# Optimization experiments

Hardware: AMD Instinct MI355X
Metric: run time of the kernel (lower is better)

The kernel has to match this reference:

```python
import jax, jax.numpy as jnp
import numpy as np

N_ATOMS = 200000
AEV_DIM = 384
H1, H2, H3 = 160, 128, 96
N_SPECIES = 4
ALPHA = 0.1  # CELU alpha used by ANI atomic networks


def setup_inputs() -> dict:
    key = jax.random.key(0)
    ks = jax.random.split(key, 8)
    aev = jax.random.normal(ks[0], (N_ATOMS, AEV_DIM), dtype=jnp.float32)
    # Disjoint species partition (matches (species==s).nonzero() buffers)
    perm = jax.random.permutation(ks[1], N_ATOMS)
    chunk = N_ATOMS // N_SPECIES
    H_idx = perm[0 * chunk:1 * chunk]
    C_idx = perm[1 * chunk:2 * chunk]
    N_idx = perm[2 * chunk:3 * chunk]
    O_idx = perm[3 * chunk:4 * chunk]

    def init(k, shape, fan_in):
        return (jax.random.normal(k, shape, dtype=jnp.float32) / np.float32(np.sqrt(fan_in)))

    # Stacked per-species MLP params: leading axis = species (H,C,N,O)
    W1 = init(ks[2], (N_SPECIES, AEV_DIM, H1), AEV_DIM); b1 = jnp.zeros((N_SPECIES, H1), jnp.float32)
    W2 = init(ks[3], (N_SPECIES, H1, H2), H1);          b2 = jnp.zeros((N_SPECIES, H2), jnp.float32)
    W3 = init(ks[4], (N_SPECIES, H2, H3), H2);          b3 = jnp.zeros((N_SPECIES, H3), jnp.float32)
    W4 = init(ks[5], (N_SPECIES, H3, 1), H3);           b4 = jnp.zeros((N_SPECIES, 1), jnp.float32)
    return {"aev": aev,
            "W1": W1, "b1": b1, "W2": W2, "b2": b2,
            "W3": W3, "b3": b3, "W4": W4, "b4": b4,
            "H_idx": H_idx, "C_idx": C_idx, "N_idx": N_idx, "O_idx": O_idx}


def _species_mlp(x, W1, b1, W2, b2, W3, b3, W4, b4):
    h = jax.nn.celu(x @ W1 + b1, ALPHA)
    h = jax.nn.celu(h @ W2 + b2, ALPHA)
    h = jax.nn.celu(h @ W3 + b3, ALPHA)
    return (h @ W4 + b4).reshape(-1)  # per-atom scalar energy


def reference(aev, W1, b1, W2, b2, W3, b3, W4, b4, H_idx, C_idx, N_idx, O_idx):
    out = jnp.zeros((aev.shape[0],), dtype=aev.dtype)
    # Fixed small loop over the 4 species networks (structurally distinct experts)
    for s, idx in enumerate((H_idx, C_idx, N_idx, O_idx)):
        e = _species_mlp(aev[idx], W1[s], b1[s], W2[s], b2[s], W3[s], b3[s], W4[s], b4[s])
        out = out.at[idx].add(e)  # index_add_ scatter
    # output.unsqueeze(0).sum(dim=1) -> molecular energy, shape [1]
    return out[None, :].sum(axis=1)
```

## Files before the change

kernel.cpp:

```cpp
#include <hip/hip_runtime.h>

#define DI __device__ __forceinline__

constexpr int AEV = 384;
constexpr int H1N = 160;
constexpr int H2N = 128;
constexpr int H3N = 96;
constexpr int NSP = 4;
constexpr int W1P = 200;
constexpr int W2P = 168;
constexpr int W3P = 136;
constexpr int W3OFF = H2N * W2P;

using half8  = __attribute__((ext_vector_type(8))) _Float16;
using half4v = __attribute__((ext_vector_type(4))) _Float16;
using f32x4  = __attribute__((ext_vector_type(4))) float;

__device__ __align__(16) _Float16 g_w1[NSP * H1N * AEV];
__device__ __align__(16) _Float16 g_w2[NSP * H2N * H1N];
__device__ __align__(16) _Float16 g_w3[NSP * H3N * H2N];

DI float celu_f(float x) {
  return fmaxf(x, 0.f) + 0.1f * (exp2f(fminf(x, 0.f) * 14.426950408889634f) - 1.f);
}
DI f32x4 mfma16h(half8 a, half8 b, f32x4 c) {
  return __builtin_amdgcn_mfma_f32_16x16x32_f16(a, b, c, 0, 0, 0);
}
DI half8 cvt8(float4 a, float4 b) {
  half8 t;
  t[0] = (_Float16)a.x; t[1] = (_Float16)a.y; t[2] = (_Float16)a.z; t[3] = (_Float16)a.w;
  t[4] = (_Float16)b.x; t[5] = (_Float16)b.y; t[6] = (_Float16)b.z; t[7] = (_Float16)b.w;
  return t;
}
DI half4v shfl4(half4v v, int src) {
  union { half4v h; int i[2]; } u;
  u.h = v;
  u.i[0] = __shfl(u.i[0], src, 64);
  u.i[1] = __shfl(u.i[1], src, 64);
  return u.h;
}
DI half8 bfrag(const half4v* hb, int ks, int l15, int quad) {
  const int sLo = (quad & 1) * 32 + l15, sHi = sLo + 16;
  half4v loA = shfl4(hb[2 * ks], sLo),     loB = shfl4(hb[2 * ks + 1], sLo);
  half4v hiA = shfl4(hb[2 * ks], sHi),     hiB = shfl4(hb[2 * ks + 1], sHi);
  half4v lo = (quad & 2) ? loB : loA;
  half4v hi = (quad & 2) ? hiB : hiA;
  half8 b;
  b[0] = lo[0]; b[1] = lo[1]; b[2] = lo[2]; b[3] = lo[3];
  b[4] = hi[0]; b[5] = hi[1]; b[6] = hi[2]; b[7] = hi[3];
  return b;
}

template <int K, int N>
DI void tp(const float* __restrict__ src, _Float16* dst, int id) {
  constexpr int per = K * N;
  int s = id / per, r = id % per;
  int n = r / K, k = r % K;
  dst[s * per + n * K + k] = (_Float16)src[s * per + k * N + n];
}

__global__ void prep(const float* __restrict__ W1, const float* __restrict__ W2,
                     const float* __restrict__ W3, float* __restrict__ out) {
  int id = blockIdx.x * 256 + threadIdx.x;
  if (id == 0) out[0] = 0.f;
  constexpr int E1 = NSP * AEV * H1N;
  constexpr int E2 = NSP * H1N * H2N;
  constexpr int E3 = NSP * H2N * H3N;
  if (id < E1)                 tp<AEV, H1N>(W1, g_w1, id);
  else if (id < E1 + E2)       tp<H1N, H2N>(W2, g_w2, id - E1);
  else if (id < E1 + E2 + E3)  tp<H2N, H3N>(W3, g_w3, id - E1 - E2);
}

__global__ __launch_bounds__(512, 4) void fused_mlp(
    const float* __restrict__ aev,
    const float* __restrict__ b1, const float* __restrict__ b2,
    const float* __restrict__ b3,
    const float* __restrict__ W4, const float* __restrict__ pb4,
    const int* __restrict__ i0, const int* __restrict__ i1,
    const int* __restrict__ i2, const int* __restrict__ i3,
    int chunk, float* __restrict__ out) {
  __shared__ __align__(16) _Float16 WS[34560];
  __shared__ float RED[8];

  const int tid  = threadIdx.x;
  const int lane = tid & 63, wav = tid >> 6;
  const int l15  = lane & 15, quad = lane >> 4;
  const int s    = blockIdx.y;
  const int* idx = (s == 0) ? i0 : (s == 1) ? i1 : (s == 2) ? i2 : i3;

  const int a = blockIdx.x * 128 + wav * 16 + l15;
  const bool valid = (a < chunk);
  const int r = idx[valid ? a : (chunk - 1)];
  const float* xr = aev + (size_t)r * AEV + quad * 8;

  const _Float16* w1src = g_w1 + (size_t)s * H1N * AEV;

#pragma unroll
  for (int i = 0; i < 8; ++i) {
    int c = tid + i * 512;
    if (c < H1N * 24) {
      int n = c / 24, kc = c % 24;
      *(half8*)(WS + n * W1P + kc * 8) = *(const half8*)(w1src + n * AEV + kc * 8);
    }
  }
  __syncthreads();

  f32x4 acc[10];
#pragma unroll
  for (int m = 0; m < 10; ++m)
#pragma unroll
    for (int i = 0; i < 4; ++i) acc[m][i] = 0.f;

  float4 xf0 = *(const float4*)(xr), xf1 = *(const float4*)(xr + 4);
#pragma unroll
  for (int ks = 0; ks < 6; ++ks) {
    half8 bv = cvt8(xf0, xf1);
    xf0 = *(const float4*)(xr + (ks + 1) * 32);
    xf1 = *(const float4*)(xr + (ks + 1) * 32 + 4);
#pragma unroll
    for (int mt = 0; mt < 10; ++mt) {
      half8 aw = *(const half8*)(WS + (mt * 16 + l15) * W1P + ks * 32 + quad * 8);
      acc[mt] = mfma16h(aw, bv, acc[mt]);
    }
  }
  __syncthreads();
#pragma unroll
  for (int i = 0; i < 8; ++i) {
    int c = tid + i * 512;
    if (c < H1N * 24) {
      int n = c / 24, kc = c % 24;
      *(half8*)(WS + n * W1P + kc * 8) = *(const half8*)(w1src + 192 + n * AEV + kc * 8);
    }
  }
  __syncthreads();
#pragma unroll
  for (int ks = 6; ks < 12; ++ks) {
    half8 bv = cvt8(xf0, xf1);
    if (ks < 11) {
      xf0 = *(const float4*)(xr + (ks + 1) * 32);
      xf1 = *(const float4*)(xr + (ks + 1) * 32 + 4);
    }
#pragma unroll
    for (int mt = 0; mt < 10; ++mt) {
      half8 aw = *(const half8*)(WS + (mt * 16 + l15) * W1P + (ks - 6) * 32 + quad * 8);
      acc[mt] = mfma16h(aw, bv, acc[mt]);
    }
  }
  half4v hb[10];
#pragma unroll
  for (int mt = 0; mt < 10; ++mt) {
    float4 bb = *(const float4*)(b1 + s * H1N + mt * 16 + quad * 4);
    half4v o;
    o[0] = (_Float16)celu_f(acc[mt][0] + bb.x);
    o[1] = (_Float16)celu_f(acc[mt][1] + bb.y);
    o[2] = (_Float16)celu_f(acc[mt][2] + bb.z);
    o[3] = (_Float16)celu_f(acc[mt][3] + bb.w);
    hb[mt] = o;
  }

  __syncthreads();
  {
    const _Float16* w2src = g_w2 + (size_t)s * H2N * H1N;
    const _Float16* w3src = g_w3 + (size_t)s * H3N * H2N;
#pragma unroll
    for (int i = 0; i < 5; ++i) {
      int c = tid + i * 512;
      int n = c / 20, kc = c % 20;
      *(half8*)(WS + n * W2P + kc * 8) = *(const half8*)(w2src + n * H1N + kc * 8);
    }
#pragma unroll
    for (int i = 0; i < 3; ++i) {
      int c = tid + i * 512;
      int n = c / 16, kc = c % 16;
      *(half8*)(WS + W3OFF + n * W3P + kc * 8) = *(const half8*)(w3src + n * H2N + kc * 8);
    }
  }
  __syncthreads();

  f32x4 acc2[8];
#pragma unroll
  for (int m = 0; m < 8; ++m)
#pragma unroll
    for (int i = 0; i < 4; ++i) acc2[m][i] = 0.f;
#pragma unroll
  for (int ks = 0; ks < 5; ++ks) {
    half8 bv = bfrag(hb, ks, l15, quad);
#pragma unroll
    for (int mt = 0; mt < 8; ++mt) {
      half8 aw = *(const half8*)(WS + (mt * 16 + l15) * W2P + ks * 32 + quad * 8);
      acc2[mt] = mfma16h(aw, bv, acc2[mt]);
    }
  }
  half4v hb2[8];
#pragma unroll
  for (int mt = 0; mt < 8; ++mt) {
    float4 bb = *(const float4*)(b2 + s * H2N + mt * 16 + quad * 4);
    half4v o;
    o[0] = (_Float16)celu_f(acc2[mt][0] + bb.x);
    o[1] = (_Float16)celu_f(acc2[mt][1] + bb.y);
    o[2] = (_Float16)celu_f(acc2[mt][2] + bb.z);
    o[3] = (_Float16)celu_f(acc2[mt][3] + bb.w);
    hb2[mt] = o;
  }

  f32x4 acc3[6];
#pragma unroll
  for (int m = 0; m < 6; ++m)
#pragma unroll
    for (int i = 0; i < 4; ++i) acc3[m][i] = 0.f;
#pragma unroll
  for (int ks = 0; ks < 4; ++ks) {
    half8 bv = bfrag(hb2, ks, l15, quad);
#pragma unroll
    for (int mt = 0; mt < 6; ++mt) {
      half8 aw = *(const half8*)(WS + W3OFF + (mt * 16 + l15) * W3P + ks * 32 + quad * 8);
      acc3[mt] = mfma16h(aw, bv, acc3[mt]);
    }
  }

  float e = 0.f;
#pragma unroll
  for (int mt = 0; mt < 6; ++mt) {
    float4 bb = *(const float4*)(b3 + s * H3N + mt * 16 + quad * 4);
    float4 wv = *(const float4*)(W4 + s * H3N + mt * 16 + quad * 4);
    e += (float)(_Float16)celu_f(acc3[mt][0] + bb.x) * wv.x
       + (float)(_Float16)celu_f(acc3[mt][1] + bb.y) * wv.y
       + (float)(_Float16)celu_f(acc3[mt][2] + bb.z) * wv.z
       + (float)(_Float16)celu_f(acc3[mt][3] + bb.w) * wv.w;
  }
  e += __shfl_xor(e, 16, 64);
  e += __shfl_xor(e, 32, 64);
  e = (lane < 16 && valid) ? (e + pb4[s]) : 0.f;
#pragma unroll
  for (int off = 1; off < 64; off <<= 1) e += __shfl_xor(e, off, 64);
  if (lane == 0) RED[wav] = e;
  __syncthreads();
  if (tid == 0) {
    float t = 0.f;
#pragma unroll
    for (int i = 0; i < 8; ++i) t += RED[i];
    atomicAdd(out, t);
  }
}

extern "C" void kernel_launch(void* const* d_in, const int* in_sizes, int n_in,
                              void* d_out, int out_size, void* d_ws, size_t ws_size,
                              hipStream_t stream) {
  (void)n_in; (void)d_ws; (void)ws_size; (void)out_size;
  const float* aev = (const float*)d_in[0];
  const float* W1  = (const float*)d_in[1];
  const float* b1  = (const float*)d_in[2];
  const float* W2  = (const float*)d_in[3];
  const float* b2  = (const float*)d_in[4];
  const float* W3  = (const float*)d_in[5];
  const float* b3  = (const float*)d_in[6];
  const float* W4  = (const float*)d_in[7];
  const float* b4  = (const float*)d_in[8];
  const int* iH = (const int*)d_in[9];
  const int* iC = (const int*)d_in[10];
  const int* iN = (const int*)d_in[11];
  const int* iO = (const int*)d_in[12];
  const int chunk = in_sizes[9];

  constexpr int TOT = NSP * (AEV * H1N + H1N * H2N + H2N * H3N);
  prep<<<TOT / 256, 256, 0, stream>>>(W1, W2, W3, (float*)d_out);

  const int tiles = (chunk + 127) / 128;
  fused_mlp<<<dim3(tiles, NSP), 512, 0, stream>>>(aev, b1, b2, b3, W4, b4,
                                                  iH, iC, iN, iO, chunk, (float*)d_out);
}
```

Before: 477.5 us.

## Make MLP kernel persistent with resident W1 and cross-tile AEV prefetch

Switches to a persistent grid of 64 blocks per species that loop over 128-atom tiles. The full W1 slice stays resident in LDS for the whole block. W2 and W3 are restaged in a shared region each iteration. The next tile's AEV rows are prefetched with nontemporal loads during layers 2-3, and the atomic add happens once per block. This removes the per-tile W1 reload, the launch overhead, and the exposed gather latency. In exchange it drops occupancy to 2 blocks per CU, adds more barriers per tile, and reloads W2/W3 from global memory every tile.

```diff
diff --git a/kernel.cpp b/kernel.cpp
--- a/kernel.cpp
+++ b/kernel.cpp
@@ -7,10 +7,13 @@
 constexpr int H2N = 128;
 constexpr int H3N = 96;
 constexpr int NSP = 4;
-constexpr int W1P = 200;
-constexpr int W2P = 168;
-constexpr int W3P = 136;
-constexpr int W3OFF = H2N * W2P;
+
+constexpr int W1P  = 392;
+constexpr int W2AP = 104;
+constexpr int W2BP = 72;
+constexpr int W3P  = 136;
+constexpr int RH   = H1N * W1P;
+constexpr int WSH  = RH + H2N * W2AP;
 
 using half8  = __attribute__((ext_vector_type(8))) _Float16;
 using half4v = __attribute__((ext_vector_type(4))) _Float16;
@@ -26,10 +29,10 @@
 DI f32x4 mfma16h(half8 a, half8 b, f32x4 c) {
   return __builtin_amdgcn_mfma_f32_16x16x32_f16(a, b, c, 0, 0, 0);
 }
-DI half8 cvt8(float4 a, float4 b) {
+DI half8 cvt8(f32x4 a, f32x4 b) {
   half8 t;
-  t[0] = (_Float16)a.x; t[1] = (_Float16)a.y; t[2] = (_Float16)a.z; t[3] = (_Float16)a.w;
-  t[4] = (_Float16)b.x; t[5] = (_Float16)b.y; t[6] = (_Float16)b.z; t[7] = (_Float16)b.w;
+  t[0] = (_Float16)a[0]; t[1] = (_Float16)a[1]; t[2] = (_Float16)a[2]; t[3] = (_Float16)a[3];
+  t[4] = (_Float16)b[0]; t[5] = (_Float16)b[1]; t[6] = (_Float16)b[2]; t[7] = (_Float16)b[3];
   return t;
 }
 DI half4v shfl4(half4v v, int src) {
@@ -50,6 +53,7 @@
   b[4] = hi[0]; b[5] = hi[1]; b[6] = hi[2]; b[7] = hi[3];
   return b;
 }
+DI f32x4 ntl4(const float* p) { return __builtin_nontemporal_load((const f32x4*)p); }
 
 template <int K, int N>
 DI void tp(const float* __restrict__ src, _Float16* dst, int id) {
@@ -71,7 +75,7 @@
   else if (id < E1 + E2 + E3)  tp<H2N, H3N>(W3, g_w3, id - E1 - E2);
 }
 
-__global__ __launch_bounds__(512, 4) void fused_mlp(
+__global__ __launch_bounds__(512, 2) void fused_mlp(
     const float* __restrict__ aev,
     const float* __restrict__ b1, const float* __restrict__ b2,
     const float* __restrict__ b3,
@@ -79,7 +83,7 @@
     const int* __restrict__ i0, const int* __restrict__ i1,
     const int* __restrict__ i2, const int* __restrict__ i3,
     int chunk, float* __restrict__ out) {
-  __shared__ __align__(16) _Float16 WS[34560];
+  __shared__ __align__(16) _Float16 WS[WSH];
   __shared__ float RED[8];
 
   const int tid  = threadIdx.x;
@@ -87,160 +91,188 @@
   const int l15  = lane & 15, quad = lane >> 4;
   const int s    = blockIdx.y;
   const int* idx = (s == 0) ? i0 : (s == 1) ? i1 : (s == 2) ? i2 : i3;
-
-  const int a = blockIdx.x * 128 + wav * 16 + l15;
-  const bool valid = (a < chunk);
-  const int r = idx[valid ? a : (chunk - 1)];
-  const float* xr = aev + (size_t)r * AEV + quad * 8;
+  const int ntiles = (chunk + 127) >> 7;
 
   const _Float16* w1src = g_w1 + (size_t)s * H1N * AEV;
-
-#pragma unroll
-  for (int i = 0; i < 8; ++i) {
+  const _Float16* w2src = g_w2 + (size_t)s * H2N * H1N;
+  const _Float16* w3src = g_w3 + (size_t)s * H3N * H2N;
+
+#pragma unroll
+  for (int i = 0; i < 15; ++i) {
     int c = tid + i * 512;
-    if (c < H1N * 24) {
-      int n = c / 24, kc = c % 24;
-      *(half8*)(WS + n * W1P + kc * 8) = *(const half8*)(w1src + n * AEV + kc * 8);
-    }
+    int n = c / 48, kc = c % 48;
+    *(half8*)(WS + n * W1P + kc * 8) = *(const half8*)(w1src + n * AEV + kc * 8);
   }
+
+  int t = blockIdx.x;
+  bool valid;
+  const float* xr;
+  {
+    int a = t * 128 + wav * 16 + l15;
+    valid = (a < chunk);
+    int r = idx[valid ? a : (chunk - 1)];
+    xr = aev + (size_t)r * AEV + quad * 8;
+  }
+  f32x4 pA0 = ntl4(xr),      pB0 = ntl4(xr + 4);
+  f32x4 pA1 = ntl4(xr + 32), pB1 = ntl4(xr + 36);
+  f32x4 pA2 = ntl4(xr + 64), pB2 = ntl4(xr + 68);
+  f32x4 pA3 = ntl4(xr + 96), pB3 = ntl4(xr + 100);
+
+  float bsum = 0.f;
   __syncthreads();
 
-  f32x4 acc[10];
-#pragma unroll
-  for (int m = 0; m < 10; ++m)
-#pragma unroll
-    for (int i = 0; i < 4; ++i) acc[m][i] = 0.f;
-
-  float4 xf0 = *(const float4*)(xr), xf1 = *(const float4*)(xr + 4);
-#pragma unroll
-  for (int ks = 0; ks < 6; ++ks) {
-    half8 bv = cvt8(xf0, xf1);
-    xf0 = *(const float4*)(xr + (ks + 1) * 32);
-    xf1 = *(const float4*)(xr + (ks + 1) * 32 + 4);
+  for (; t < ntiles; t += 64) {
+    f32x4 acc[10];
+#pragma unroll
+    for (int m = 0; m < 10; ++m)
+#pragma unroll
+      for (int i = 0; i < 4; ++i) acc[m][i] = 0.f;
+#pragma unroll
+    for (int ks = 0; ks < 12; ++ks) {
+      half8 bv = cvt8(pA0, pB0);
+      pA0 = pA1; pB0 = pB1; pA1 = pA2; pB1 = pB2; pA2 = pA3; pB2 = pB3;
+      if (ks < 8) {
+        pA3 = ntl4(xr + (ks + 4) * 32);
+        pB3 = ntl4(xr + (ks + 4) * 32 + 4);
+      }
+#pragma unroll
+      for (int mt = 0; mt < 10; ++mt) {
+        half8 aw = *(const half8*)(WS + (mt * 16 + l15) * W1P + ks * 32 + quad * 8);
+        acc[mt] = mfma16h(aw, bv, acc[mt]);
+      }
+    }
+    half4v hb[10];
 #pragma unroll
     for (int mt = 0; mt < 10; ++mt) {
-      half8 aw = *(const half8*)(WS + (mt * 16 + l15) * W1P + ks * 32 + quad * 8);
-      acc[mt] = mfma16h(aw, bv, acc[mt]);
-    }
+      float4 bb = *(const float4*)(b1 + s * H1N + mt * 16 + quad * 4);
+      half4v o;
+      o[0] = (_Float16)celu_f(acc[mt][0] + bb.x);
+      o[1] = (_Float16)celu_f(acc[mt][1] + bb.y);
+      o[2] = (_Float16)celu_f(acc[mt][2] + bb.z);
+      o[3] = (_Float16)celu_f(acc[mt][3] + bb.w);
+      hb[mt] = o;
+    }
+
+    bool v2;
+    const float* xr2;
+    {
+      int a2 = (t + 64) * 128 + wav * 16 + l15;
+      v2 = (a2 < chunk);
+      int r2 = idx[v2 ? a2 : (chunk - 1)];
+      xr2 = aev + (size_t)r2 * AEV + quad * 8;
+    }
+    const int nA0 = tid / 12,          kA0 = tid % 12;
+    const int nA1 = (tid + 512) / 12,  kA1 = (tid + 512) % 12;
+    const int nA2 = (tid + 1024) / 12, kA2 = (tid + 1024) % 12;
+    half8 sA0 = *(const half8*)(w2src + nA0 * H1N + kA0 * 8);
+    half8 sA1 = *(const half8*)(w2src + nA1 * H1N + kA1 * 8);
+    half8 sA2 = *(const half8*)(w2src + nA2 * H1N + kA2 * 8);
+    pA0 = ntl4(xr2);      pB0 = ntl4(xr2 + 4);
+    pA1 = ntl4(xr2 + 32); pB1 = ntl4(xr2 + 36);
+    pA2 = ntl4(xr2 + 64); pB2 = ntl4(xr2 + 68);
+    pA3 = ntl4(xr2 + 96); pB3 = ntl4(xr2 + 100);
+    *(half8*)(WS + RH + nA0 * W2AP + kA0 * 8) = sA0;
+    *(half8*)(WS + RH + nA1 * W2AP + kA1 * 8) = sA1;
+    *(half8*)(WS + RH + nA2 * W2AP + kA2 * 8) = sA2;
+    __syncthreads();
+
+    f32x4 acc2[8];
+#pragma unroll
+    for (int m = 0; m < 8; ++m)
+#pragma unroll
+      for (int i = 0; i < 4; ++i) acc2[m][i] = 0.f;
+#pragma unroll
+    for (int ks = 0; ks < 3; ++ks) {
+      half8 bv = bfrag(hb, ks, l15, quad);
+#pragma unroll
+      for (int mt = 0; mt < 8; ++mt) {
+        half8 aw = *(const half8*)(WS + RH + (mt * 16 + l15) * W2AP + ks * 32 + quad * 8);
+        acc2[mt] = mfma16h(aw, bv, acc2[mt]);
+      }
+    }
+    const int nB0 = tid / 8,         kB0 = tid % 8;
+    const int nB1 = (tid + 512) / 8, kB1 = (tid + 512) % 8;
+    half8 sB0 = *(const half8*)(w2src + 96 + nB0 * H1N + kB0 * 8);
+    half8 sB1 = *(const half8*)(w2src + 96 + nB1 * H1N + kB1 * 8);
+    __syncthreads();
+    *(half8*)(WS + RH + nB0 * W2BP + kB0 * 8) = sB0;
+    *(half8*)(WS + RH + nB1 * W2BP + kB1 * 8) = sB1;
+    __syncthreads();
+
+#pragma unroll
+    for (int ks = 3; ks < 5; ++ks) {
+      half8 bv = bfrag(hb, ks, l15, quad);
+#pragma unroll
+      for (int mt = 0; mt < 8; ++mt) {
+        half8 aw = *(const half8*)(WS + RH + (mt * 16 + l15) * W2BP + (ks - 3) * 32 + quad * 8);
+        acc2[mt] = mfma16h(aw, bv, acc2[mt]);
+      }
+    }
+    half4v hb2[8];
+#pragma unroll
+    for (int mt = 0; mt < 8; ++mt) {
+      float4 bb = *(const float4*)(b2 + s * H2N + mt * 16 + quad * 4);
+      half4v o;
+      o[0] = (_Float16)celu_f(acc2[mt][0] + bb.x);
+      o[1] = (_Float16)celu_f(acc2[mt][1] + bb.y);
+      o[2] = (_Float16)celu_f(acc2[mt][2] + bb.z);
+      o[3] = (_Float16)celu_f(acc2[mt][3] + bb.w);
+      hb2[mt] = o;
+    }
+    const int nC0 = tid / 16,          kC0 = tid % 16;
+    const int nC1 = (tid + 512) / 16,  kC1 = (tid + 512) % 16;
+    const int nC2 = (tid + 1024) / 16, kC2 = (tid + 1024) % 16;
+    half8 sC0 = *(const half8*)(w3src + nC0 * H2N + kC0 * 8);
+    half8 sC1 = *(const half8*)(w3src + nC1 * H2N + kC1 * 8);
+    half8 sC2 = *(const half8*)(w3src + nC2 * H2N + kC2 * 8);
+    __syncthreads();
+    *(half8*)(WS + RH + nC0 * W3P + kC0 * 8) = sC0;
+    *(half8*)(WS + RH + nC1 * W3P + kC1 * 8) = sC1;
+    *(half8*)(WS + RH + nC2 * W3P + kC2 * 8) = sC2;
+    __syncthreads();
+
+    f32x4 acc3[6];
+#pragma unroll
+    for (int m = 0; m < 6; ++m)
+#pragma unroll
+      for (int i = 0; i < 4; ++i) acc3[m][i] = 0.f;
+#pragma unroll
+    for (int ks = 0; ks < 4; ++ks) {
+      half8 bv = bfrag(hb2, ks, l15, quad);
+#pragma unroll
+      for (int mt = 0; mt < 6; ++mt) {
+        half8 aw = *(const half8*)(WS + RH + (mt * 16 + l15) * W3P + ks * 32 + quad * 8);
+        acc3[mt] = mfma16h(aw, bv, acc3[mt]);
+      }
+    }
+
+    float e = 0.f;
+#pragma unroll
+    for (int mt = 0; mt < 6; ++mt) {
+      float4 bb = *(const float4*)(b3 + s * H3N + mt * 16 + quad * 4);
+      float4 wv = *(const float4*)(W4 + s * H3N + mt * 16 + quad * 4);
+      e += (float)(_Float16)celu_f(acc3[mt][0] + bb.x) * wv.x
+         + (float)(_Float16)celu_f(acc3[mt][1] + bb.y) * wv.y
+         + (float)(_Float16)celu_f(acc3[mt][2] + bb.z) * wv.z
+         + (float)(_Float16)celu_f(acc3[mt][3] + bb.w) * wv.w;
+    }
+    e += __shfl_xor(e, 16, 64);
+    e += __shfl_xor(e, 32, 64);
+    e = (lane < 16 && valid) ? (e + pb4[s]) : 0.f;
+#pragma unroll
+    for (int off = 1; off < 64; off <<= 1) e += __shfl_xor(e, off, 64);
+    if (lane == 0) RED[wav] = e;
+    __syncthreads();
+    if (tid == 0) {
+      float ts = 0.f;
+#pragma unroll
+      for (int i = 0; i < 8; ++i) ts += RED[i];
+      bsum += ts;
+    }
+    valid = v2;
+    xr = xr2;
   }
-  __syncthreads();
-#pragma unroll
-  for (int i = 0; i < 8; ++i) {
-    int c = tid + i * 512;
-    if (c < H1N * 24) {
-      int n = c / 24, kc = c % 24;
-      *(half8*)(WS + n * W1P + kc * 8) = *(const half8*)(w1src + 192 + n * AEV + kc * 8);
-    }
-  }
-  __syncthreads();
-#pragma unroll
-  for (int ks = 6; ks < 12; ++ks) {
-    half8 bv = cvt8(xf0, xf1);
-    if (ks < 11) {
-      xf0 = *(const float4*)(xr + (ks + 1) * 32);
-      xf1 = *(const float4*)(xr + (ks + 1) * 32 + 4);
-    }
-#pragma unroll
-    for (int mt = 0; mt < 10; ++mt) {
-      half8 aw = *(const half8*)(WS + (mt * 16 + l15) * W1P + (ks - 6) * 32 + quad * 8);
-      acc[mt] = mfma16h(aw, bv, acc[mt]);
-    }
-  }
-  half4v hb[10];
-#pragma unroll
-  for (int mt = 0; mt < 10; ++mt) {
-    float4 bb = *(const float4*)(b1 + s * H1N + mt * 16 + quad * 4);
-    half4v o;
-    o[0] = (_Float16)celu_f(acc[mt][0] + bb.x);
-    o[1] = (_Float16)celu_f(acc[mt][1] + bb.y);
-    o[2] = (_Float16)celu_f(acc[mt][2] + bb.z);
-    o[3] = (_Float16)celu_f(acc[mt][3] + bb.w);
-    hb[mt] = o;
-  }
-
-  __syncthreads();
-  {
-    const _Float16* w2src = g_w2 + (size_t)s * H2N * H1N;
-    const _Float16* w3src = g_w3 + (size_t)s * H3N * H2N;
-#pragma unroll
-    for (int i = 0; i < 5; ++i) {
-      int c = tid + i * 512;
-      int n = c / 20, kc = c % 20;
-      *(half8*)(WS + n * W2P + kc * 8) = *(const half8*)(w2src + n * H1N + kc * 8);
-    }
-#pragma unroll
-    for (int i = 0; i < 3; ++i) {
-      int c = tid + i * 512;
-      int n = c / 16, kc = c % 16;
-      *(half8*)(WS + W3OFF + n * W3P + kc * 8) = *(const half8*)(w3src + n * H2N + kc * 8);
-    }
-  }
-  __syncthreads();
-
-  f32x4 acc2[8];
-#pragma unroll
-  for (int m = 0; m < 8; ++m)
-#pragma unroll
-    for (int i = 0; i < 4; ++i) acc2[m][i] = 0.f;
-#pragma unroll
-  for (int ks = 0; ks < 5; ++ks) {
-    half8 bv = bfrag(hb, ks, l15, quad);
-#pragma unroll
-    for (int mt = 0; mt < 8; ++mt) {
-      half8 aw = *(const half8*)(WS + (mt * 16 + l15) * W2P + ks * 32 + quad * 8);
-      acc2[mt] = mfma16h(aw, bv, acc2[mt]);
-    }
-  }
-  half4v hb2[8];
-#pragma unroll
-  for (int mt = 0; mt < 8; ++mt) {
-    float4 bb = *(const float4*)(b2 + s * H2N + mt * 16 + quad * 4);
-    half4v o;
-    o[0] = (_Float16)celu_f(acc2[mt][0] + bb.x);
-    o[1] = (_Float16)celu_f(acc2[mt][1] + bb.y);
-    o[2] = (_Float16)celu_f(acc2[mt][2] + bb.z);
-    o[3] = (_Float16)celu_f(acc2[mt][3] + bb.w);
-    hb2[mt] = o;
-  }
-
-  f32x4 acc3[6];
-#pragma unroll
-  for (int m = 0; m < 6; ++m)
-#pragma unroll
-    for (int i = 0; i < 4; ++i) acc3[m][i] = 0.f;
-#pragma unroll
-  for (int ks = 0; ks < 4; ++ks) {
-    half8 bv = bfrag(hb2, ks, l15, quad);
-#pragma unroll
-    for (int mt = 0; mt < 6; ++mt) {
-      half8 aw = *(const half8*)(WS + W3OFF + (mt * 16 + l15) * W3P + ks * 32 + quad * 8);
-      acc3[mt] = mfma16h(aw, bv, acc3[mt]);
-    }
-  }
-
-  float e = 0.f;
-#pragma unroll
-  for (int mt = 0; mt < 6; ++mt) {
-    float4 bb = *(const float4*)(b3 + s * H3N + mt * 16 + quad * 4);
-    float4 wv = *(const float4*)(W4 + s * H3N + mt * 16 + quad * 4);
-    e += (float)(_Float16)celu_f(acc3[mt][0] + bb.x) * wv.x
-       + (float)(_Float16)celu_f(acc3[mt][1] + bb.y) * wv.y
-       + (float)(_Float16)celu_f(acc3[mt][2] + bb.z) * wv.z
-       + (float)(_Float16)celu_f(acc3[mt][3] + bb.w) * wv.w;
-  }
-  e += __shfl_xor(e, 16, 64);
-  e += __shfl_xor(e, 32, 64);
-  e = (lane < 16 && valid) ? (e + pb4[s]) : 0.f;
-#pragma unroll
-  for (int off = 1; off < 64; off <<= 1) e += __shfl_xor(e, off, 64);
-  if (lane == 0) RED[wav] = e;
-  __syncthreads();
-  if (tid == 0) {
-    float t = 0.f;
-#pragma unroll
-    for (int i = 0; i < 8; ++i) t += RED[i];
-    atomicAdd(out, t);
-  }
+  if (tid == 0) atomicAdd(out, bsum);
 }
 
 extern "C" void kernel_launch(void* const* d_in, const int* in_sizes, int n_in,
@@ -265,7 +297,6 @@
   constexpr int TOT = NSP * (AEV * H1N + H1N * H2N + H2N * H3N);
   prep<<<TOT / 256, 256, 0, stream>>>(W1, W2, W3, (float*)d_out);
 
-  const int tiles = (chunk + 127) / 128;
-  fused_mlp<<<dim3(tiles, NSP), 512, 0, stream>>>(aev, b1, b2, b3, W4, b4,
-                                                  iH, iC, iN, iO, chunk, (float*)d_out);
-}
+  fused_mlp<<<dim3(64, NSP), 512, 0, stream>>>(aev, b1, b2, b3, W4, b4,
+                                               iH, iC, iN, iO, chunk, (float*)d_out);
+}
```

New measurement: 500.5 us. 1.05x slower.
